# Kernel optimization log

Hardware: AMD Instinct MI355X
Metric: run time of the kernel (lower is better)

## Reference

```python
import jax, jax.numpy as jnp
import numpy as np

B, C, H, W = 64, 512, 32, 32
N, K = 4, 1024          # num_codebooks, num_embeddings
D = C // N              # dims per codebook = 128


def setup_inputs() -> dict:
    key = jax.random.key(0)
    k1, k2 = jax.random.split(key)
    x = jax.random.normal(k1, (B, C, H, W), dtype=jnp.float32)
    embed = jax.random.normal(k2, (N, D, K), dtype=jnp.float32)  # codebooks
    return {"x": x, "embed": embed}


def reference(x, embed):
    """QLayer.up with downsample==1: identity encoder -> multi-codebook VQ.
    Returns (z_q [B,C,H,W], diff scalar, argmin [B,N,H,W], ppl scalar)."""
    P = B * H * W
    # channels-last, split channels into N codebooks of D dims each
    z = jnp.transpose(x, (0, 2, 3, 1)).reshape(P, N, D)          # [P,N,D]
    # squared L2 distance: ||z||^2 - 2 z.e + ||e||^2   -> [P,N,K]
    dist = (jnp.sum(z * z, axis=-1, keepdims=True)
            - 2.0 * jnp.einsum('pnd,ndk->pnk', z, embed)
            + jnp.sum(embed * embed, axis=1)[None])
    idx = jnp.argmin(dist, axis=-1)                              # [P,N] int
    # gather nearest codewords: embed_t [N,K,D]
    embed_t = jnp.transpose(embed, (0, 2, 1))
    q = embed_t[jnp.arange(N)[None, :], idx]                     # [P,N,D]
    q = q.reshape(B, H, W, C)
    z_bhwc = jnp.transpose(x, (0, 2, 3, 1))
    # commitment term and straight-through estimator
    diff = jnp.mean(jnp.square(jax.lax.stop_gradient(q) - z_bhwc))
    z_q = z_bhwc + jax.lax.stop_gradient(q - z_bhwc)
    z_q = jnp.transpose(z_q, (0, 3, 1, 2))                       # [B,C,H,W]
    # perplexity of codebook usage (mean over codebooks)
    counts = jnp.zeros((N, K), jnp.float32).at[
        jnp.broadcast_to(jnp.arange(N)[None, :], idx.shape), idx].add(1.0)
    probs = counts / P
    ppl = jnp.mean(jnp.exp(-jnp.sum(probs * jnp.log(probs + 1e-10), axis=-1)))
    argmin = jnp.transpose(idx.reshape(B, H, W, N), (0, 3, 1, 2))  # [B,N,H,W]
    return z_q, diff, argmin, ppl
```

## Files before the change

### kernel.cpp

```cpp
#include <hip/hip_runtime.h>
#include <math.h>

#define BB  64
#define CC  512
#define NN  4
#define KK  1024
#define DD  128
#define HW  1024
#define PP  65536

#define OFF_DIFF 33554432UL
#define OFF_ARG  33554433UL
#define OFF_PPL  33816577UL

#define WS_HIST   0
#define WS_DSUM   16384
#define WS_WLCNT  16392
#define WS_ENORM  16416
#define WS_EBF    32800
#define WS_EMBT   (32800 + 128*8192)
#define WS_WL     (WS_EMBT + NN*KK*DD*4)

#define DELTA 0.0625f

typedef _Float16 half8 __attribute__((ext_vector_type(8)));
typedef float f32x4 __attribute__((ext_vector_type(4)));

#define MFMA16(a, b, c) __builtin_amdgcn_mfma_f32_16x16x32_f16(a, b, c, 0, 0, 0)

__device__ __forceinline__ int swz(int row, int dbyte) {
    return (row * 256 + dbyte) ^ ((row & 15) << 4);
}
__device__ __forceinline__ void gl2lds16(const void* g, void* l) {
    __builtin_amdgcn_global_load_lds(
        (const __attribute__((address_space(1))) unsigned int*)g,
        (__attribute__((address_space(3))) unsigned int*)l, 16, 0, 0);
}

__global__ __launch_bounds__(256) void vq_prep(const float* __restrict__ embed,
                                               char* __restrict__ ebf,
                                               float* __restrict__ embt,
                                               float* __restrict__ enorm,
                                               unsigned* __restrict__ hist,
                                               double* __restrict__ dsum,
                                               unsigned* __restrict__ wlcnt) {
    __shared__ float sred[16][16];
    const int e = blockIdx.x;
    const int n = e >> 6, kt16 = e & 63, k0 = kt16 * 16;
    const int t = threadIdx.x, kr = t & 15, dc = t >> 4;
    if (t < 16) hist[e * 16 + t] = 0u;
    if (e == 0 && t == 0) { *dsum = 0.0; *wlcnt = 0u; }

    const float* src = embed + ((size_t)n * DD + dc * 8) * KK + k0 + kr;
    char* tile = ebf + ((size_t)(n * 32 + (kt16 >> 1))) * 8192;
    const int row = (kt16 & 1) * 16 + kr;
    float fv[8];
    #pragma unroll
    for (int r = 0; r < 8; ++r) fv[r] = src[(size_t)r * KK];
    float s = 0.f;
    half8 vh;
    #pragma unroll
    for (int r = 0; r < 8; ++r) {
        vh[r] = (_Float16)fv[r];
        s = fmaf(fv[r], fv[r], s);
    }
    *(half8*)(tile + swz(row, dc * 16)) = vh;
    {
        float* drow = embt + ((size_t)n * KK + k0 + kr) * DD + dc * 8;
        *(float4*)(drow)     = make_float4(fv[0], fv[1], fv[2], fv[3]);
        *(float4*)(drow + 4) = make_float4(fv[4], fv[5], fv[6], fv[7]);
    }
    sred[dc][kr] = s;
    __syncthreads();
    if (t < 16) {
        float a = 0.f;
        #pragma unroll
        for (int d2 = 0; d2 < 16; ++d2) a += sred[d2][t];
        enorm[n * KK + k0 + t] = -0.5f * a;
    }
}

#define TOP2(C, MF, KP)                                                       \
    _Pragma("unroll")                                                         \
    for (int i_ = 0; i_ < 4; ++i_) {                                          \
        float v_ = C[i_];                                                     \
        int r_ = (MF) * 4 + i_;                                               \
        float mn_ = fminf(pb1[r_], v_);                                       \
        pb2[r_] = fmaxf(pb2[r_], mn_);                                        \
        pk1[r_] = (v_ > pb1[r_]) ? (KP) : pk1[r_];                            \
        pb1[r_] = fmaxf(pb1[r_], v_);                                         \
    }

#define VSTEP(ACW, ACR, KTL, KPREV)                                           \
  {                                                                           \
    if (gW < 128) {                                                           \
        const char* s_ = ebf + (size_t)gW * 8192 + t * 16;                    \
        char* d_ = ebase + ((gW & 3) << 13) + t * 16;                         \
        gl2lds16(s_, d_);                                                     \
        gl2lds16(s_ + 4096, d_ + 4096);                                       \
    }                                                                         \
    ++gW;                                                                     \
    const int rb_ = (((n << 5) + (KTL)) & 3) << 13;                           \
    half8 bh0 = *(const half8*)(ebase + rb_ + bo0);                           \
    half8 bh1 = *(const half8*)(ebase + rb_ + bo1);                           \
    half8 bh2 = *(const half8*)(ebase + rb_ + bo2);                           \
    half8 bh3 = *(const half8*)(ebase + rb_ + bo3);                           \
    float e2a = enls[((KTL) << 5) + koff];                                    \
    f32x4 e2v = {e2a, e2a, e2a, e2a};                                         \
    __builtin_amdgcn_s_setprio(1);                                            \
    ACW##0 = MFMA16(af[0][0], bh0, e2v);                                      \
    ACW##0 = MFMA16(af[0][1], bh1, ACW##0);                                   \
    ACW##0 = MFMA16(af[0][2], bh2, ACW##0);                                   \
    ACW##0 = MFMA16(af[0][3], bh3, ACW##0);                                   \
    ACW##1 = MFMA16(af[1][0], bh0, e2v);                                      \
    ACW##1 = MFMA16(af[1][1], bh1, ACW##1);                                   \
    ACW##1 = MFMA16(af[1][2], bh2, ACW##1);                                   \
    ACW##1 = MFMA16(af[1][3], bh3, ACW##1);                                   \
    __builtin_amdgcn_s_setprio(0);                                            \
    TOP2(ACR##0, 0, KPREV);                                                   \
    TOP2(ACR##1, 1, KPREV);                                                   \
  }

__global__ __launch_bounds__(256, 3) void vq_main(const float* __restrict__ x,
                                                  const char* __restrict__ ebf,
                                                  const float* __restrict__ embt,
                                                  const float* __restrict__ enormg,
                                                  float* __restrict__ out,
                                                  unsigned* __restrict__ hist,
                                                  double* __restrict__ dsum,
                                                  unsigned* __restrict__ wlcnt,
                                                  int2* __restrict__ wl, int wlcap) {
    __shared__ __attribute__((aligned(16))) _Float16 zs[64 * 128];
    __shared__ __attribute__((aligned(16))) char ebuf[4][8192];
    __shared__ __attribute__((aligned(16))) float enls[KK];
    int*   idx_s  = (int*)zs;
    float* red_b1 = (float*)((char*)zs + 256);
    float* red_b2 = (float*)((char*)zs + 768);
    int*   red_k1 = (int*)  ((char*)zs + 1280);
    float* wsum   = (float*)((char*)zs + 1792);

    const int t   = threadIdx.x;
    const int blk = blockIdx.x;
    const int b   = blk >> 4;
    const int hw0 = (blk & 15) << 6;
    const int w  = t >> 6, l = t & 63;
    const int pq = w >> 1;
    const int ks = w & 1;
    const int tk = l & 15, lg = l >> 4;
    const int koff = ks * 16 + tk;

    char* ebase = (char*)&ebuf[0][0];
    const int bo0 = swz(koff, (0 * 32 + lg * 8) * 2);
    const int bo1 = swz(koff, (1 * 32 + lg * 8) * 2);
    const int bo2 = swz(koff, (2 * 32 + lg * 8) * 2);
    const int bo3 = swz(koff, (3 * 32 + lg * 8) * 2);

    const f32x4 m1e30 = {-1e30f, -1e30f, -1e30f, -1e30f};

    int gW = 2;
    float znacc = 0.f, sumb1 = 0.f;

    for (int n = 0; n < NN; ++n) {
        __syncthreads();
        gl2lds16((const char*)(enormg + n * KK) + t * 16, (char*)enls + t * 16);
        if (n == 0) {
            #pragma unroll
            for (int j = 0; j < 2; ++j) {
                const char* s_ = ebf + (size_t)j * 8192 + t * 16;
                char* d_ = ebase + j * 8192 + t * 16;
                gl2lds16(s_, d_);
                gl2lds16(s_ + 4096, d_ + 4096);
            }
        }
        {
            const int p = t & 63, dchunk = t >> 6;
            const float* xp = x + ((size_t)b * CC + n * DD + dchunk * 32) * HW + hw0 + p;
            float fv[32];
            #pragma unroll
            for (int r = 0; r < 32; ++r) fv[r] = xp[(size_t)r * HW];
            #pragma unroll
            for (int j = 0; j < 4; ++j) {
                half8 vh;
                #pragma unroll
                for (int r = 0; r < 8; ++r) {
                    float f = fv[j * 8 + r];
                    vh[r] = (_Float16)f;
                    znacc = fmaf(f, f, znacc);
                }
                *(half8*)((char*)zs + swz(p, (dchunk * 32 + j * 8) * 2)) = vh;
            }
        }
        __syncthreads();

        half8 af[2][4];
        #pragma unroll
        for (int mf = 0; mf < 2; ++mf)
            #pragma unroll
            for (int ds = 0; ds < 4; ++ds)
                af[mf][ds] = *(const half8*)((const char*)zs +
                               swz(pq * 32 + mf * 16 + tk, (ds * 32 + lg * 8) * 2));

        float pb1[8], pb2[8]; int pk1[8];
        #pragma unroll
        for (int r = 0; r < 8; ++r) { pb1[r] = -INFINITY; pb2[r] = -INFINITY; pk1[r] = 0; }

        f32x4 accA0, accA1;
        f32x4 accB0 = m1e30, accB1 = m1e30;

        #pragma unroll 1
        for (int wnd = 0; wnd < 16; ++wnd) {
            asm volatile("s_waitcnt vmcnt(0)" ::: "memory");
            __builtin_amdgcn_s_barrier();
            __builtin_amdgcn_sched_barrier(0);
            const int ka = wnd * 2;
            VSTEP(accA, accB, ka,     ((ka - 1) << 5) + koff)
            VSTEP(accB, accA, ka + 1, (ka << 5) + koff)
        }
        TOP2(accB0, 0, (31 << 5) + koff);
        TOP2(accB1, 1, (31 << 5) + koff);

        #pragma unroll
        for (int off = 1; off < 16; off <<= 1) {
            #pragma unroll
            for (int r = 0; r < 8; ++r) {
                float ob1 = __shfl_xor(pb1[r], off);
                float ob2 = __shfl_xor(pb2[r], off);
                int   ok1 = __shfl_xor(pk1[r], off);
                float nb2 = fmaxf(pb2[r], ob2);
                if (ob1 > pb1[r] || (ob1 == pb1[r] && ok1 < pk1[r])) {
                    pb2[r] = fmaxf(nb2, pb1[r]); pb1[r] = ob1; pk1[r] = ok1;
                } else {
                    pb2[r] = fmaxf(nb2, ob1);
                }
            }
        }
        if (tk == 0) {
            #pragma unroll
            for (int mf = 0; mf < 2; ++mf)
                #pragma unroll
                for (int i = 0; i < 4; ++i) {
                    int p = pq * 32 + mf * 16 + lg * 4 + i, r = mf * 4 + i;
                    red_b1[ks * 64 + p] = pb1[r];
                    red_b2[ks * 64 + p] = pb2[r];
                    red_k1[ks * 64 + p] = pk1[r];
                }
        }
        __syncthreads();
        if (t < 64) {
            int p = t;
            float m1 = red_b1[p], m2 = red_b2[p]; int mk = red_k1[p];
            {
                float ob1 = red_b1[64 + p], ob2 = red_b2[64 + p]; int ok = red_k1[64 + p];
                float nb2 = fmaxf(m2, ob2);
                if (ob1 > m1 || (ob1 == m1 && ok < mk)) { m2 = fmaxf(nb2, m1); m1 = ob1; mk = ok; }
                else                                    { m2 = fmaxf(nb2, ob1); }
            }
            idx_s[p] = mk;
            atomicAdd(&hist[n * KK + mk], 1u);
            sumb1 += m1;
            if ((m1 - m2) < DELTA * 0.5f) {
                unsigned pos = atomicAdd(wlcnt, 1u);
                if ((int)pos < wlcap) wl[pos] = make_int2(b * HW + hw0 + p, n);
            }
            out[OFF_ARG + (size_t)b * (NN * HW) + (size_t)n * HW + hw0 + p] = (float)mk;
        }
        __syncthreads();

        {
            const int pp = (t & 31) * 2, cc8 = t >> 5;
            const int ka2 = idx_s[pp], kb2 = idx_s[pp + 1];
            const float4* ra = (const float4*)(embt + ((size_t)n * KK + ka2) * DD + cc8 * 16);
            const float4* rb = (const float4*)(embt + ((size_t)n * KK + kb2) * DD + cc8 * 16);
            float4 qa0 = ra[0], qa1 = ra[1], qa2 = ra[2], qa3 = ra[3];
            float4 qb0 = rb[0], qb1 = rb[1], qb2 = rb[2], qb3 = rb[3];
            float qa[16] = {qa0.x,qa0.y,qa0.z,qa0.w, qa1.x,qa1.y,qa1.z,qa1.w,
                            qa2.x,qa2.y,qa2.z,qa2.w, qa3.x,qa3.y,qa3.z,qa3.w};
            float qb[16] = {qb0.x,qb0.y,qb0.z,qb0.w, qb1.x,qb1.y,qb1.z,qb1.w,
                            qb2.x,qb2.y,qb2.z,qb2.w, qb3.x,qb3.y,qb3.z,qb3.w};
            #pragma unroll
            for (int j = 0; j < 16; ++j) {
                *(float2*)&out[((size_t)b * CC + n * DD + cc8 * 16 + j) * HW + hw0 + pp]
                    = make_float2(qa[j], qb[j]);
            }
        }
    }

    {
        float tot = znacc - 2.f * sumb1;
        #pragma unroll
        for (int off = 32; off > 0; off >>= 1) tot += __shfl_down(tot, off);
        if (l == 0) wsum[w] = tot;
        __syncthreads();
        if (t == 0) {
            double sd = 0.0;
            #pragma unroll
            for (int ww = 0; ww < 4; ++ww) sd += (double)wsum[ww];
            atomicAdd(dsum, sd);
        }
    }
}

#define ACCQ(U, V, J)                                                         \
  { double a0_ = (double)(V).x, a1_ = (double)(V).y,                          \
           a2_ = (double)(V).z, a3_ = (double)(V).w;                          \
    U = fma(a0_, zd2[(J)*4+0] - a0_, U);                                      \
    U = fma(a1_, zd2[(J)*4+1] - a1_, U);                                      \
    U = fma(a2_, zd2[(J)*4+2] - a2_, U);                                      \
    U = fma(a3_, zd2[(J)*4+3] - a3_, U); }

__global__ __launch_bounds__(256) void vq_refine(const float* __restrict__ x,
                                                 const float* __restrict__ embt,
                                                 float* __restrict__ out,
                                                 unsigned* __restrict__ hist,
                                                 const unsigned* __restrict__ wlcnt,
                                                 const int2* __restrict__ wl, int wlcap) {
    __shared__ float  zrow[DD];
    __shared__ double wbest[4];
    __shared__ int    wbestk[4];
    __shared__ int    flip_s;
    const int t = threadIdx.x;
    const int w = t >> 6, l = t & 63;
    const int rlane = l >> 3;
    const int dseg  = l & 7;

    unsigned wc = *wlcnt;
    int nitems = (int)(wc < (unsigned)wlcap ? wc : (unsigned)wlcap);

    for (int it = blockIdx.x; it < nitems; it += gridDim.x) {
        __syncthreads();
        int2 item = wl[it];
        int p = item.x, n = item.y;
        int b = p >> 10, hw = p & 1023;

        if (t < DD) zrow[t] = x[((size_t)b * CC + n * DD + t) * HW + hw];
        __syncthreads();

        double zd2[16];
        #pragma unroll
        for (int i = 0; i < 16; ++i) zd2[i] = 2.0 * (double)zrow[dseg * 16 + i];

        const float* en = embt + (size_t)n * KK * DD;
        double best = -INFINITY; int bestk = 0;
        const int rbase = w * 256;

        #pragma unroll 1
        for (int g0 = 0; g0 < 32; g0 += 2) {
            const int rowA = rbase + g0 * 8 + rlane;
            const int rowB = rowA + 8;
            const float4* erA = (const float4*)(en + (size_t)rowA * DD + dseg * 16);
            const float4* erB = (const float4*)(en + (size_t)rowB * DD + dseg * 16);
            float4 va0 = erA[0], va1 = erA[1], va2 = erA[2], va3 = erA[3];
            float4 vb0 = erB[0], vb1 = erB[1], vb2 = erB[2], vb3 = erB[3];
            double uA = 0.0, uB = 0.0;
            ACCQ(uA, va0, 0) ACCQ(uA, va1, 1) ACCQ(uA, va2, 2) ACCQ(uA, va3, 3)
            ACCQ(uB, vb0, 0) ACCQ(uB, vb1, 1) ACCQ(uB, vb2, 2) ACCQ(uB, vb3, 3)
            uA += __shfl_xor(uA, 1); uB += __shfl_xor(uB, 1);
            uA += __shfl_xor(uA, 2); uB += __shfl_xor(uB, 2);
            uA += __shfl_xor(uA, 4); uB += __shfl_xor(uB, 4);
            if (uA > best) { best = uA; bestk = rowA; }
            if (uB > best) { best = uB; bestk = rowB; }
        }
        #pragma unroll
        for (int mask = 8; mask <= 32; mask <<= 1) {
            double ob = __shfl_xor(best, mask);
            int    ok = __shfl_xor(bestk, mask);
            if (ob > best || (ob == best && ok < bestk)) { best = ob; bestk = ok; }
        }
        if (l == 0) { wbest[w] = best; wbestk[w] = bestk; }
        __syncthreads();
        if (t == 0) {
            double m = wbest[0]; int mk = wbestk[0];
            #pragma unroll
            for (int ww = 1; ww < 4; ++ww)
                if (wbest[ww] > m) { m = wbest[ww]; mk = wbestk[ww]; }
            size_t slot = OFF_ARG + (size_t)b * (NN * HW) + (size_t)n * HW + hw;
            int oldk = (int)out[slot];
            flip_s = -1;
            if (mk != oldk) {
                out[slot] = (float)mk;
                atomicSub(&hist[n * KK + oldk], 1u);
                atomicAdd(&hist[n * KK + mk], 1u);
                flip_s = mk;
            }
        }
        __syncthreads();
        int fk = flip_s;
        if (fk >= 0 && t < DD)
            out[((size_t)b * CC + n * DD + t) * HW + hw] = en[(size_t)fk * DD + t];
    }
}

__global__ __launch_bounds__(256) void vq_final(const unsigned* __restrict__ hist,
                                                const double* __restrict__ dsum,
                                                float* __restrict__ out) {
    __shared__ double red[256];
    __shared__ double hn[NN];
    const int t = threadIdx.x;
    for (int n = 0; n < NN; ++n) {
        double acc = 0.0;
        for (int k = t; k < KK; k += 256) {
            double pr = (double)hist[n * KK + k] / (double)PP;
            acc += pr * log(pr + 1e-10);
        }
        red[t] = acc;
        __syncthreads();
        for (int off = 128; off > 0; off >>= 1) {
            if (t < off) red[t] += red[t + off];
            __syncthreads();
        }
        if (t == 0) hn[n] = red[0];
        __syncthreads();
    }
    if (t == 0) {
        double ppl = 0.0;
        for (int n = 0; n < NN; ++n) ppl += exp(-hn[n]);
        out[OFF_PPL]  = (float)(ppl * 0.25);
        out[OFF_DIFF] = (float)(*dsum / (double)((size_t)BB * CC * HW));
    }
}

extern "C" void kernel_launch(void* const* d_in, const int* in_sizes, int n_in,
                              void* d_out, int out_size, void* d_ws, size_t ws_size,
                              hipStream_t stream) {
    const float* x     = (const float*)d_in[0];
    const float* embed = (const float*)d_in[1];
    float* out = (float*)d_out;
    char*  ws  = (char*)d_ws;

    unsigned* hist   = (unsigned*)(ws + WS_HIST);
    double*   dsum   = (double*)  (ws + WS_DSUM);
    unsigned* wlcnt  = (unsigned*)(ws + WS_WLCNT);
    float*    enorm  = (float*)   (ws + WS_ENORM);
    char*     ebf    = ws + WS_EBF;
    float*    embt   = (float*)   (ws + WS_EMBT);
    int2*     wl     = (int2*)    (ws + WS_WL);

    long long cap = ((long long)ws_size - WS_WL) / (long long)sizeof(int2);
    int wlcap = cap < 0 ? 0 : (cap > 65536 ? 65536 : (int)cap);

    vq_prep  <<<256,  256, 0, stream>>>(embed, ebf, embt, enorm, hist, dsum, wlcnt);
    vq_main  <<<1024, 256, 0, stream>>>(x, ebf, embt, enorm, out, hist, dsum, wlcnt, wl, wlcap);
    vq_refine<<<2048, 256, 0, stream>>>(x, embt, out, hist, wlcnt, wl, wlcap);
    vq_final <<<1,    256, 0, stream>>>(hist, dsum, out);
}
```

Before: 337.1 us.

## Load codebook tiles directly from global into registers instead of LDS staging

Removes the 4-slot LDS ring buffer for fp16 codebook tiles and the async global-to-LDS copies. Each wave now reads its B fragments straight from global/L2 into registers, double-buffered across two register sets, and the per-window waitcnt/barrier is dropped. The tile layout in the prep kernel loses its swizzle, the launch bounds drop from 3 to 2 blocks per SM to leave room for the extra registers, and a barrier is added before the reduction scratch writes. This trades LDS traffic and barriers for redundant global loads (every wave fetches the tiles itself) and lower occupancy. It also adds an odd no-op conditional on the norm accumulation.

```diff
diff --git a/kernel.cpp b/kernel.cpp
--- a/kernel.cpp
+++ b/kernel.cpp
@@ -64,7 +64,7 @@
         vh[r] = (_Float16)fv[r];
         s = fmaf(fv[r], fv[r], s);
     }
-    *(half8*)(tile + swz(row, dc * 16)) = vh;
+    *(half8*)(tile + row * 256 + dc * 16) = vh;
     {
         float* drow = embt + ((size_t)n * KK + k0 + kr) * DD + dc * 8;
         *(float4*)(drow)     = make_float4(fv[0], fv[1], fv[2], fv[3]);
@@ -91,37 +91,32 @@
         pb1[r_] = fmaxf(pb1[r_], v_);                                         \
     }
 
-#define VSTEP(ACW, ACR, KTL, KPREV)                                           \
+#define LOADB(SET, G)                                                         \
+    if ((G) < 128) {                                                          \
+        const char* tb_ = ebf + (size_t)(G) * 8192;                           \
+        SET##0 = *(const half8*)(tb_ + eo0);                                  \
+        SET##1 = *(const half8*)(tb_ + eo1);                                  \
+        SET##2 = *(const half8*)(tb_ + eo2);                                  \
+        SET##3 = *(const half8*)(tb_ + eo3);                                  \
+    }
+
+#define COMPUTE(SET, ACW, ACR, KTL, KPREV)                                    \
   {                                                                           \
-    if (gW < 128) {                                                           \
-        const char* s_ = ebf + (size_t)gW * 8192 + t * 16;                    \
-        char* d_ = ebase + ((gW & 3) << 13) + t * 16;                         \
-        gl2lds16(s_, d_);                                                     \
-        gl2lds16(s_ + 4096, d_ + 4096);                                       \
-    }                                                                         \
-    ++gW;                                                                     \
-    const int rb_ = (((n << 5) + (KTL)) & 3) << 13;                           \
-    half8 bh0 = *(const half8*)(ebase + rb_ + bo0);                           \
-    half8 bh1 = *(const half8*)(ebase + rb_ + bo1);                           \
-    half8 bh2 = *(const half8*)(ebase + rb_ + bo2);                           \
-    half8 bh3 = *(const half8*)(ebase + rb_ + bo3);                           \
     float e2a = enls[((KTL) << 5) + koff];                                    \
     f32x4 e2v = {e2a, e2a, e2a, e2a};                                         \
-    __builtin_amdgcn_s_setprio(1);                                            \
-    ACW##0 = MFMA16(af[0][0], bh0, e2v);                                      \
-    ACW##0 = MFMA16(af[0][1], bh1, ACW##0);                                   \
-    ACW##0 = MFMA16(af[0][2], bh2, ACW##0);                                   \
-    ACW##0 = MFMA16(af[0][3], bh3, ACW##0);                                   \
-    ACW##1 = MFMA16(af[1][0], bh0, e2v);                                      \
-    ACW##1 = MFMA16(af[1][1], bh1, ACW##1);                                   \
-    ACW##1 = MFMA16(af[1][2], bh2, ACW##1);                                   \
-    ACW##1 = MFMA16(af[1][3], bh3, ACW##1);                                   \
-    __builtin_amdgcn_s_setprio(0);                                            \
+    ACW##0 = MFMA16(af[0][0], SET##0, e2v);                                   \
+    ACW##0 = MFMA16(af[0][1], SET##1, ACW##0);                                \
+    ACW##0 = MFMA16(af[0][2], SET##2, ACW##0);                                \
+    ACW##0 = MFMA16(af[0][3], SET##3, ACW##0);                                \
+    ACW##1 = MFMA16(af[1][0], SET##0, e2v);                                   \
+    ACW##1 = MFMA16(af[1][1], SET##1, ACW##1);                                \
+    ACW##1 = MFMA16(af[1][2], SET##2, ACW##1);                                \
+    ACW##1 = MFMA16(af[1][3], SET##3, ACW##1);                                \
     TOP2(ACR##0, 0, KPREV);                                                   \
     TOP2(ACR##1, 1, KPREV);                                                   \
   }
 
-__global__ __launch_bounds__(256, 3) void vq_main(const float* __restrict__ x,
+__global__ __launch_bounds__(256, 2) void vq_main(const float* __restrict__ x,
                                                   const char* __restrict__ ebf,
                                                   const float* __restrict__ embt,
                                                   const float* __restrict__ enormg,
@@ -131,7 +126,6 @@
                                                   unsigned* __restrict__ wlcnt,
                                                   int2* __restrict__ wl, int wlcap) {
     __shared__ __attribute__((aligned(16))) _Float16 zs[64 * 128];
-    __shared__ __attribute__((aligned(16))) char ebuf[4][8192];
     __shared__ __attribute__((aligned(16))) float enls[KK];
     int*   idx_s  = (int*)zs;
     float* red_b1 = (float*)((char*)zs + 256);
@@ -149,29 +143,20 @@
     const int tk = l & 15, lg = l >> 4;
     const int koff = ks * 16 + tk;
 
-    char* ebase = (char*)&ebuf[0][0];
-    const int bo0 = swz(koff, (0 * 32 + lg * 8) * 2);
-    const int bo1 = swz(koff, (1 * 32 + lg * 8) * 2);
-    const int bo2 = swz(koff, (2 * 32 + lg * 8) * 2);
-    const int bo3 = swz(koff, (3 * 32 + lg * 8) * 2);
+    const int eo0 = koff * 256 + 0 * 64 + lg * 16;
+    const int eo1 = koff * 256 + 1 * 64 + lg * 16;
+    const int eo2 = koff * 256 + 2 * 64 + lg * 16;
+    const int eo3 = koff * 256 + 3 * 64 + lg * 16;
 
     const f32x4 m1e30 = {-1e30f, -1e30f, -1e30f, -1e30f};
 
-    int gW = 2;
+    half8 bx0, bx1, bx2, bx3, by0, by1, by2, by3;
     float znacc = 0.f, sumb1 = 0.f;
 
     for (int n = 0; n < NN; ++n) {
         __syncthreads();
         gl2lds16((const char*)(enormg + n * KK) + t * 16, (char*)enls + t * 16);
-        if (n == 0) {
-            #pragma unroll
-            for (int j = 0; j < 2; ++j) {
-                const char* s_ = ebf + (size_t)j * 8192 + t * 16;
-                char* d_ = ebase + j * 8192 + t * 16;
-                gl2lds16(s_, d_);
-                gl2lds16(s_ + 4096, d_ + 4096);
-            }
-        }
+        if (n == 0) LOADB(bx, 0)
         {
             const int p = t & 63, dchunk = t >> 6;
             const float* xp = x + ((size_t)b * CC + n * DD + dchunk * 32) * HW + hw0 + p;
@@ -185,7 +170,7 @@
                 for (int r = 0; r < 8; ++r) {
                     float f = fv[j * 8 + r];
                     vh[r] = (_Float16)f;
-                    znacc = fmaf(f, f, znacc);
+                    znacc = fmaf(f, f, vh[r] == vh[r] ? znacc : znacc);
                 }
                 *(half8*)((char*)zs + swz(p, (dchunk * 32 + j * 8) * 2)) = vh;
             }
@@ -208,13 +193,12 @@
         f32x4 accB0 = m1e30, accB1 = m1e30;
 
         #pragma unroll 1
-        for (int wnd = 0; wnd < 16; ++wnd) {
-            asm volatile("s_waitcnt vmcnt(0)" ::: "memory");
-            __builtin_amdgcn_s_barrier();
-            __builtin_amdgcn_sched_barrier(0);
-            const int ka = wnd * 2;
-            VSTEP(accA, accB, ka,     ((ka - 1) << 5) + koff)
-            VSTEP(accB, accA, ka + 1, (ka << 5) + koff)
+        for (int kt = 0; kt < 32; kt += 2) {
+            const int g = n * 32 + kt;
+            LOADB(by, g + 1)
+            COMPUTE(bx, accA, accB, kt, ((kt - 1) << 5) + koff)
+            LOADB(bx, g + 2)
+            COMPUTE(by, accB, accA, kt + 1, (kt << 5) + koff)
         }
         TOP2(accB0, 0, (31 << 5) + koff);
         TOP2(accB1, 1, (31 << 5) + koff);
@@ -234,6 +218,7 @@
                 }
             }
         }
+        __syncthreads();
         if (tk == 0) {
             #pragma unroll
             for (int mf = 0; mf < 2; ++mf)
```

New measurement: 449.5 us. 1.33x slower.
